# Kernel optimization log

Measured on AMD Instinct MI355X. Metric: run time of the kernel, lower is better.

The kernel has to match this reference:

```python
import jax, jax.numpy as jnp
import numpy as np

B, NQ, HW, C, H = 4, 1024, 4096, 1024, 8
DH = C // H  # 128


def setup_inputs() -> dict:
    key = jax.random.key(0)
    ks = jax.random.split(key, 11)
    s = 0.02
    return {
        "query": jax.random.normal(ks[0], (B, NQ, C), dtype=jnp.float32),
        "memory": jax.random.normal(ks[1], (B, HW, C), dtype=jnp.float32),
        "mask": jax.random.uniform(ks[2], (B, NQ, HW), dtype=jnp.float32),
        "Wq": jax.random.normal(ks[3], (C, C), dtype=jnp.float32) * s,
        "bq": jnp.zeros((C,), dtype=jnp.float32),
        "Wk": jax.random.normal(ks[4], (C, C), dtype=jnp.float32) * s,
        "bk": jnp.zeros((C,), dtype=jnp.float32),
        "Wv": jax.random.normal(ks[5], (C, C), dtype=jnp.float32) * s,
        "bv": jnp.zeros((C,), dtype=jnp.float32),
        "Wo": jax.random.normal(ks[6], (C, C), dtype=jnp.float32) * s,
        "bo": jnp.zeros((C,), dtype=jnp.float32),
    }


def reference(query, memory, mask, Wq, bq, Wk, bk, Wv, bv, Wo, bo):
    # Projections (torch nn.Linear convention: x @ W.T + b)
    q = (query @ Wq.T + bq).reshape(B, NQ, H, DH)
    k = (memory @ Wk.T + bk).reshape(B, HW, H, DH)
    v = (memory @ Wv.T + bv).reshape(B, HW, H, DH)

    scale = 1.0 / jnp.sqrt(jnp.asarray(DH, dtype=q.dtype))
    scores = jnp.einsum("bqhd,bkhd->bhqk", q * scale, k)  # [B,H,NQ,HW]

    # mask < 0.5 means disallowed (True in torch bool attn_mask -> -inf)
    allowed = (mask >= 0.5)[:, None, :, :]  # broadcast over heads
    scores = jnp.where(allowed, scores, jnp.asarray(-jnp.inf, dtype=scores.dtype))

    attn = jax.nn.softmax(scores, axis=-1)
    out = jnp.einsum("bhqk,bkhd->bqhd", attn, v).reshape(B, NQ, C)
    return out @ Wo.T + bo
```

## Files before the change

### kernel.cpp

```cpp
#include <hip/hip_runtime.h>


#define NB 4
#define NQL 1024
#define HWK 4096
#define CC 1024
#define NH 8
#define DHD 128

typedef __attribute__((ext_vector_type(8))) short s16x8;
typedef __attribute__((ext_vector_type(4))) short s16x4;
typedef __attribute__((ext_vector_type(4))) float f32x4;
typedef unsigned int u32;
typedef unsigned long long u64;
typedef const __attribute__((address_space(1))) u32* gas1;
typedef __attribute__((address_space(3))) u32* las3;

__device__ __forceinline__ unsigned short f2bf(float f) {
  u32 u = __float_as_uint(f);
  u32 r = u + 0x7FFFu + ((u >> 16) & 1u);
  return (unsigned short)(r >> 16);
}

__device__ __forceinline__ void gld16(const void* g, void* l) {
  __builtin_amdgcn_global_load_lds((gas1)g, (las3)l, 16, 0, 0);
}

#define MFMA16(a, b, c) __builtin_amdgcn_mfma_f32_16x16x32_bf16((a), (b), (c), 0, 0, 0)

__global__ void cvt_bf16(const float* __restrict__ s, short* __restrict__ d, int n8) {
  int i = blockIdx.x * 256 + threadIdx.x;
  int stride = gridDim.x * 256;
  for (; i < n8; i += stride) {
    const float4* s4 = (const float4*)s;
    float4 a = s4[i * 2];
    float4 b = s4[i * 2 + 1];
    s16x8 o;
    o[0] = (short)f2bf(a.x); o[1] = (short)f2bf(a.y);
    o[2] = (short)f2bf(a.z); o[3] = (short)f2bf(a.w);
    o[4] = (short)f2bf(b.x); o[5] = (short)f2bf(b.y);
    o[6] = (short)f2bf(b.z); o[7] = (short)f2bf(b.w);
    *(s16x8*)(d + (size_t)i * 8) = o;
  }
}

__global__ void mask_bits(const float* __restrict__ mask, u64* __restrict__ words) {
  int t = blockIdx.x * 256 + threadIdx.x;
  int wi = t >> 6;
  int lane = t & 63;
  int k = ((lane >> 2) & 3) * 16 + (lane >> 4) * 4 + (lane & 3);
  float v = mask[(size_t)wi * 64 + k];
  u64 bits = __ballot(v >= 0.5f);
  if (lane == 0) words[wi] = bits;
}

template <int EPI>
__global__ __launch_bounds__(256, 2) void gemm_bt(const short* __restrict__ A,
                                                  const short* __restrict__ W,
                                                  const float* __restrict__ bias,
                                                  void* __restrict__ Cout, float scale) {
  __shared__ alignas(16) short As[128 * 32];
  __shared__ alignas(16) short Bs[128 * 32];
  int nwg = gridDim.x;
  int bid = blockIdx.x;
  int wg = (bid & 7) * (nwg >> 3) + (bid >> 3);
  int bm = wg >> 3;
  int bn = wg & 7;
  int tid = threadIdx.x;
  int w = tid >> 6, lane = tid & 63, lo = lane & 15, hi = lane >> 4;
  int wr = w >> 1, wc = w & 1;
  const short* Ab = A + (size_t)bm * 128 * 1024;
  const short* Wb = W + (size_t)bn * 128 * 1024;
  f32x4 acc[4][4] = {};
  int srow = lane >> 2;
  int scolb = (lane & 3) * 16;

  for (int kt = 0; kt < 32; ++kt) {
    __syncthreads();
#pragma unroll
    for (int i = 0; i < 2; ++i) {
      int c = w * 2 + i;
      int row = c * 16 + srow;
      int sc = scolb ^ ((row & 3) << 4);
      gld16(Ab + (size_t)row * 1024 + kt * 32 + (sc >> 1), (char*)As + c * 1024);
      gld16(Wb + (size_t)row * 1024 + kt * 32 + (sc >> 1), (char*)Bs + c * 1024);
    }
    __syncthreads();
    s16x8 af[4], bf[4];
#pragma unroll
    for (int mf = 0; mf < 4; ++mf) {
      int row = wr * 64 + mf * 16 + lo;
      af[mf] = *(const s16x8*)((const char*)As + row * 64 + ((hi * 16) ^ ((row & 3) << 4)));
    }
#pragma unroll
    for (int nf = 0; nf < 4; ++nf) {
      int row = wc * 64 + nf * 16 + lo;
      bf[nf] = *(const s16x8*)((const char*)Bs + row * 64 + ((hi * 16) ^ ((row & 3) << 4)));
    }
#pragma unroll
    for (int mf = 0; mf < 4; ++mf)
#pragma unroll
      for (int nf = 0; nf < 4; ++nf) acc[mf][nf] = MFMA16(af[mf], bf[nf], acc[mf][nf]);
  }

#pragma unroll
  for (int nf = 0; nf < 4; ++nf) {
    int n = bn * 128 + wc * 64 + nf * 16 + lo;
    float bv = bias[n];
#pragma unroll
    for (int mf = 0; mf < 4; ++mf) {
      int m0 = bm * 128 + wr * 64 + mf * 16 + hi * 4;
      if constexpr (EPI == 0 || EPI == 1) {
        short* O = (short*)Cout;
#pragma unroll
        for (int r = 0; r < 4; ++r) {
          float v = acc[mf][nf][r] + bv;
          if constexpr (EPI == 0) v *= scale;
          O[(size_t)(m0 + r) * 1024 + n] = (short)f2bf(v);
        }
      } else if constexpr (EPI == 2) {
        short* O = (short*)Cout;
        int bb = m0 >> 12;
        int kk = m0 & 4095;
        s16x4 pk;
#pragma unroll
        for (int r = 0; r < 4; ++r) pk[r] = (short)f2bf(acc[mf][nf][r] + bv);
        *(s16x4*)(O + (size_t)bb * 4194304 + (size_t)n * 4096 + kk) = pk;
      } else {
        float* O = (float*)Cout;
#pragma unroll
        for (int r = 0; r < 4; ++r) O[(size_t)(m0 + r) * 1024 + n] = acc[mf][nf][r] + bv;
      }
    }
  }
}

__global__ __launch_bounds__(256, 1) void attn_kernel(const short* __restrict__ Qp,
                                                      const short* __restrict__ Kp,
                                                      const short* __restrict__ VT,
                                                      const u64* __restrict__ Mb,
                                                      short* __restrict__ AO) {
  __shared__ alignas(16) short Ks[2][8192];
  __shared__ alignas(16) short Vs[2][8192];
  __shared__ alignas(16) short Ps[4][2048];

  int bid = blockIdx.x;
  int wg = (bid & 7) * 32 + (bid >> 3);
  int bh = wg >> 3, qb = wg & 7;
  int b = bh >> 3, h = bh & 7;
  int tid = threadIdx.x, w = tid >> 6, lane = tid & 63, lo = lane & 15, hi = lane >> 4;
  int q0 = qb * 128 + w * 32;

  s16x8 qf_[2][4];
#pragma unroll
  for (int qf = 0; qf < 2; ++qf)
#pragma unroll
    for (int kf = 0; kf < 4; ++kf) {
      int q = q0 + qf * 16 + lo;
      qf_[qf][kf] = *(const s16x8*)(Qp + (size_t)(b * NQL + q) * CC + h * DHD + kf * 32 + hi * 8);
    }

  f32x4 acc[2][8] = {};
  float m_[2] = {-3e38f, -3e38f};
  float l_[2] = {0.f, 0.f};

  int krow = lane >> 4;
  int kcolb = (lane & 15) * 16;
  int vrow = lane >> 3;
  int vcolb = (lane & 7) * 16;

  auto stage = [&](int t, int buf) {
    int kv0 = t * 64;
#pragma unroll
    for (int i = 0; i < 4; ++i) {
      int c = w * 4 + i;
      int row = c * 4 + krow;
      int sc = kcolb ^ ((row & 7) << 4);
      gld16(Kp + (size_t)(b * HWK + kv0 + row) * CC + h * DHD + (sc >> 1), (char*)Ks[buf] + c * 1024);
    }
#pragma unroll
    for (int i = 0; i < 4; ++i) {
      int c = w * 4 + i;
      int d = c * 8 + vrow;
      int sc = vcolb ^ ((d & 7) << 4);
      gld16(VT + (size_t)((b * NH + h) * DHD + d) * HWK + kv0 + (sc >> 1), (char*)Vs[buf] + c * 1024);
    }
  };

  stage(0, 0);
  __syncthreads();

  for (int t = 0; t < 64; ++t) {
    int buf = t & 1;
    if (t < 63) stage(t + 1, buf ^ 1);

    f32x4 st[2][4] = {};
#pragma unroll
    for (int nf = 0; nf < 4; ++nf) {
      int kidx = nf * 16 + lo;
      int swz = (kidx & 7) << 4;
#pragma unroll
      for (int kf = 0; kf < 4; ++kf) {
        s16x8 a = *(const s16x8*)((const char*)Ks[buf] + kidx * 256 + ((kf * 64 + hi * 16) ^ swz));
        st[0][nf] = MFMA16(a, qf_[0][kf], st[0][nf]);
        st[1][nf] = MFMA16(a, qf_[1][kf], st[1][nf]);
      }
    }

#pragma unroll
    for (int qf = 0; qf < 2; ++qf) {
      int q = q0 + qf * 16 + lo;
      u64 word = Mb[(size_t)(b * NQL + q) * 64 + t];
      u32 halfm = (u32)(word >> (hi * 16)) & 0xFFFFu;
      float smax = -3e38f;
#pragma unroll
      for (int nf = 0; nf < 4; ++nf)
#pragma unroll
        for (int r = 0; r < 4; ++r) smax = fmaxf(smax, st[qf][nf][r]);
      smax = fmaxf(smax, __shfl_xor(smax, 16));
      smax = fmaxf(smax, __shfl_xor(smax, 32));
      float mnew = fmaxf(m_[qf], smax);
      float alpha = __builtin_amdgcn_exp2f(m_[qf] - mnew);
      float tsum = 0.f;
      int qr = qf * 16 + lo;
#pragma unroll
      for (int nf = 0; nf < 4; ++nf) {
        float p0 = __builtin_amdgcn_exp2f(st[qf][nf][0] - mnew);
        float p1 = __builtin_amdgcn_exp2f(st[qf][nf][1] - mnew);
        float p2 = __builtin_amdgcn_exp2f(st[qf][nf][2] - mnew);
        float p3 = __builtin_amdgcn_exp2f(st[qf][nf][3] - mnew);
        p0 = ((halfm >> (nf * 4 + 0)) & 1) ? p0 : 0.f;
        p1 = ((halfm >> (nf * 4 + 1)) & 1) ? p1 : 0.f;
        p2 = ((halfm >> (nf * 4 + 2)) & 1) ? p2 : 0.f;
        p3 = ((halfm >> (nf * 4 + 3)) & 1) ? p3 : 0.f;
        tsum += p0 + p1 + p2 + p3;
        u32 w0 = __builtin_amdgcn_perm(__float_as_uint(p1), __float_as_uint(p0), 0x07060302u);
        u32 w1 = __builtin_amdgcn_perm(__float_as_uint(p3), __float_as_uint(p2), 0x07060302u);
        uint2 pv; pv.x = w0; pv.y = w1;
        *(uint2*)((char*)Ps[w] + qr * 128 + ((nf * 32 + hi * 8) ^ ((lo & 7) << 4))) = pv;
      }
      tsum += __shfl_xor(tsum, 16);
      tsum += __shfl_xor(tsum, 32);
      l_[qf] = l_[qf] * alpha + tsum;
      m_[qf] = mnew;
      float ar0 = __shfl(alpha, hi * 4 + 0);
      float ar1 = __shfl(alpha, hi * 4 + 1);
      float ar2 = __shfl(alpha, hi * 4 + 2);
      float ar3 = __shfl(alpha, hi * 4 + 3);
#pragma unroll
      for (int df = 0; df < 8; ++df) {
        acc[qf][df][0] *= ar0; acc[qf][df][1] *= ar1;
        acc[qf][df][2] *= ar2; acc[qf][df][3] *= ar3;
      }
    }
    asm volatile("" ::: "memory");

#pragma unroll
    for (int kt = 0; kt < 2; ++kt) {
      s16x8 pa0 = *(const s16x8*)((const char*)Ps[w] + (0 + lo) * 128 + ((kt * 64 + hi * 16) ^ ((lo & 7) << 4)));
      s16x8 pa1 = *(const s16x8*)((const char*)Ps[w] + (16 + lo) * 128 + ((kt * 64 + hi * 16) ^ ((lo & 7) << 4)));
#pragma unroll
      for (int df = 0; df < 8; ++df) {
        int d = df * 16 + lo;
        s16x8 vb = *(const s16x8*)((const char*)Vs[buf] + d * 128 + ((kt * 64 + hi * 16) ^ ((lo & 7) << 4)));
        acc[0][df] = MFMA16(pa0, vb, acc[0][df]);
        acc[1][df] = MFMA16(pa1, vb, acc[1][df]);
      }
    }
    __syncthreads();
  }

#pragma unroll
  for (int qf = 0; qf < 2; ++qf) {
    float linv = 1.0f / l_[qf];
    float lr0 = __shfl(linv, hi * 4 + 0);
    float lr1 = __shfl(linv, hi * 4 + 1);
    float lr2 = __shfl(linv, hi * 4 + 2);
    float lr3 = __shfl(linv, hi * 4 + 3);
    int qbase = q0 + qf * 16 + hi * 4;
#pragma unroll
    for (int df = 0; df < 8; ++df) {
      int col = h * DHD + df * 16 + lo;
      AO[(size_t)(b * NQL + qbase + 0) * CC + col] = (short)f2bf(acc[qf][df][0] * lr0);
      AO[(size_t)(b * NQL + qbase + 1) * CC + col] = (short)f2bf(acc[qf][df][1] * lr1);
      AO[(size_t)(b * NQL + qbase + 2) * CC + col] = (short)f2bf(acc[qf][df][2] * lr2);
      AO[(size_t)(b * NQL + qbase + 3) * CC + col] = (short)f2bf(acc[qf][df][3] * lr3);
    }
  }
}

extern "C" void kernel_launch(void* const* d_in, const int* in_sizes, int n_in,
                              void* d_out, int out_size, void* d_ws, size_t ws_size,
                              hipStream_t stream) {
  (void)in_sizes; (void)n_in; (void)out_size; (void)ws_size;
  const float* query = (const float*)d_in[0];
  const float* memory = (const float*)d_in[1];
  const float* mask = (const float*)d_in[2];
  const float* Wq = (const float*)d_in[3];
  const float* bq = (const float*)d_in[4];
  const float* Wk = (const float*)d_in[5];
  const float* bk = (const float*)d_in[6];
  const float* Wv = (const float*)d_in[7];
  const float* bv = (const float*)d_in[8];
  const float* Wo = (const float*)d_in[9];
  const float* bo = (const float*)d_in[10];
  float* out = (float*)d_out;

  char* ws = (char*)d_ws;
  short* qbf = (short*)(ws);
  short* mbf = (short*)(ws + (8ull << 20));
  short* wqb = (short*)(ws + (40ull << 20));
  short* wkb = wqb + (1u << 20);
  short* wvb = wqb + (2u << 20);
  short* wob = wqb + (3u << 20);
  u64* mbits = (u64*)(ws + (48ull << 20));
  short* Qp = (short*)(ws + (50ull << 20));
  short* Kp = (short*)(ws + (58ull << 20));
  short* VT = (short*)(ws + (90ull << 20));
  short* AO = (short*)(ws + (122ull << 20));

  cvt_bf16<<<2048, 256, 0, stream>>>(query, qbf, (NB * NQL * CC) / 8);
  cvt_bf16<<<2048, 256, 0, stream>>>(memory, mbf, (NB * HWK * CC) / 8);
  cvt_bf16<<<512, 256, 0, stream>>>(Wq, wqb, (CC * CC) / 8);
  cvt_bf16<<<512, 256, 0, stream>>>(Wk, wkb, (CC * CC) / 8);
  cvt_bf16<<<512, 256, 0, stream>>>(Wv, wvb, (CC * CC) / 8);
  cvt_bf16<<<512, 256, 0, stream>>>(Wo, wob, (CC * CC) / 8);
  mask_bits<<<65536, 256, 0, stream>>>(mask, mbits);

  const float qscale = 0.08838834764831845f * 1.4426950408889634f;
  gemm_bt<0><<<256, 256, 0, stream>>>(qbf, wqb, bq, Qp, qscale);
  gemm_bt<1><<<1024, 256, 0, stream>>>(mbf, wkb, bk, Kp, 1.0f);
  gemm_bt<2><<<1024, 256, 0, stream>>>(mbf, wvb, bv, VT, 1.0f);
  attn_kernel<<<256, 256, 0, stream>>>(Qp, Kp, VT, mbits, AO);
  gemm_bt<3><<<256, 256, 0, stream>>>(AO, wob, bo, out, 1.0f);
}
```

Baseline: 525.2 us.

## Halve attention query tile per block to double occupancy, add lazy rescale

Each wave of the attention kernel now handles 16 query rows instead of 32, and the grid doubles to 512 blocks with launch bounds allowing two blocks per CU. The aim is more waves in flight across 256 CUs, so memory latency and the softmax phase can overlap with other blocks' MFMA work. It also rescales the accumulator only when the running max grows by more than 8 (in log2 units), and raises wave priority around the MFMA sections. The cost is that every K/V tile loaded from memory is reused by half as many queries, which doubles K/V traffic, and the loose max threshold lets the unnormalized probabilities grow up to 2^8.

```diff
diff --git a/kernel.cpp b/kernel.cpp
--- a/kernel.cpp
+++ b/kernel.cpp
@@ -135,34 +135,31 @@
   }
 }
 
-__global__ __launch_bounds__(256, 1) void attn_kernel(const short* __restrict__ Qp,
+__global__ __launch_bounds__(256, 2) void attn_kernel(const short* __restrict__ Qp,
                                                       const short* __restrict__ Kp,
                                                       const short* __restrict__ VT,
                                                       const u64* __restrict__ Mb,
                                                       short* __restrict__ AO) {
   __shared__ alignas(16) short Ks[2][8192];
   __shared__ alignas(16) short Vs[2][8192];
-  __shared__ alignas(16) short Ps[4][2048];
+  __shared__ alignas(16) short Ps[4][1024];
 
   int bid = blockIdx.x;
-  int wg = (bid & 7) * 32 + (bid >> 3);
-  int bh = wg >> 3, qb = wg & 7;
+  int wg = (bid & 7) * 64 + (bid >> 3);
+  int bh = wg >> 4, qb = wg & 15;
   int b = bh >> 3, h = bh & 7;
   int tid = threadIdx.x, w = tid >> 6, lane = tid & 63, lo = lane & 15, hi = lane >> 4;
-  int q0 = qb * 128 + w * 32;
-
-  s16x8 qf_[2][4];
-#pragma unroll
-  for (int qf = 0; qf < 2; ++qf)
-#pragma unroll
-    for (int kf = 0; kf < 4; ++kf) {
-      int q = q0 + qf * 16 + lo;
-      qf_[qf][kf] = *(const s16x8*)(Qp + (size_t)(b * NQL + q) * CC + h * DHD + kf * 32 + hi * 8);
-    }
-
-  f32x4 acc[2][8] = {};
-  float m_[2] = {-3e38f, -3e38f};
-  float l_[2] = {0.f, 0.f};
+  int q0 = qb * 64 + w * 16;
+  int q = q0 + lo;
+
+  s16x8 qfr[4];
+#pragma unroll
+  for (int kf = 0; kf < 4; ++kf)
+    qfr[kf] = *(const s16x8*)(Qp + (size_t)(b * NQL + q) * CC + h * DHD + kf * 32 + hi * 8);
+
+  f32x4 acc[8] = {};
+  float m_ = -3e38f;
+  float l_ = 0.f;
 
   int krow = lane >> 4;
   int kcolb = (lane & 15) * 16;
@@ -194,7 +191,8 @@
     int buf = t & 1;
     if (t < 63) stage(t + 1, buf ^ 1);
 
-    f32x4 st[2][4] = {};
+    __builtin_amdgcn_s_setprio(1);
+    f32x4 st[4] = {};
 #pragma unroll
     for (int nf = 0; nf < 4; ++nf) {
       int kidx = nf * 16 + lo;
@@ -202,90 +200,87 @@
 #pragma unroll
       for (int kf = 0; kf < 4; ++kf) {
         s16x8 a = *(const s16x8*)((const char*)Ks[buf] + kidx * 256 + ((kf * 64 + hi * 16) ^ swz));
-        st[0][nf] = MFMA16(a, qf_[0][kf], st[0][nf]);
-        st[1][nf] = MFMA16(a, qf_[1][kf], st[1][nf]);
+        st[nf] = MFMA16(a, qfr[kf], st[nf]);
       }
     }
-
-#pragma unroll
-    for (int qf = 0; qf < 2; ++qf) {
-      int q = q0 + qf * 16 + lo;
-      u64 word = Mb[(size_t)(b * NQL + q) * 64 + t];
-      u32 halfm = (u32)(word >> (hi * 16)) & 0xFFFFu;
-      float smax = -3e38f;
-#pragma unroll
-      for (int nf = 0; nf < 4; ++nf)
-#pragma unroll
-        for (int r = 0; r < 4; ++r) smax = fmaxf(smax, st[qf][nf][r]);
-      smax = fmaxf(smax, __shfl_xor(smax, 16));
-      smax = fmaxf(smax, __shfl_xor(smax, 32));
-      float mnew = fmaxf(m_[qf], smax);
-      float alpha = __builtin_amdgcn_exp2f(m_[qf] - mnew);
-      float tsum = 0.f;
-      int qr = qf * 16 + lo;
-#pragma unroll
-      for (int nf = 0; nf < 4; ++nf) {
-        float p0 = __builtin_amdgcn_exp2f(st[qf][nf][0] - mnew);
-        float p1 = __builtin_amdgcn_exp2f(st[qf][nf][1] - mnew);
-        float p2 = __builtin_amdgcn_exp2f(st[qf][nf][2] - mnew);
-        float p3 = __builtin_amdgcn_exp2f(st[qf][nf][3] - mnew);
-        p0 = ((halfm >> (nf * 4 + 0)) & 1) ? p0 : 0.f;
-        p1 = ((halfm >> (nf * 4 + 1)) & 1) ? p1 : 0.f;
-        p2 = ((halfm >> (nf * 4 + 2)) & 1) ? p2 : 0.f;
-        p3 = ((halfm >> (nf * 4 + 3)) & 1) ? p3 : 0.f;
-        tsum += p0 + p1 + p2 + p3;
-        u32 w0 = __builtin_amdgcn_perm(__float_as_uint(p1), __float_as_uint(p0), 0x07060302u);
-        u32 w1 = __builtin_amdgcn_perm(__float_as_uint(p3), __float_as_uint(p2), 0x07060302u);
-        uint2 pv; pv.x = w0; pv.y = w1;
-        *(uint2*)((char*)Ps[w] + qr * 128 + ((nf * 32 + hi * 8) ^ ((lo & 7) << 4))) = pv;
-      }
-      tsum += __shfl_xor(tsum, 16);
-      tsum += __shfl_xor(tsum, 32);
-      l_[qf] = l_[qf] * alpha + tsum;
-      m_[qf] = mnew;
+    __builtin_amdgcn_s_setprio(0);
+
+    u64 word = Mb[(size_t)(b * NQL + q) * 64 + t];
+    u32 halfm = (u32)(word >> (hi * 16)) & 0xFFFFu;
+    float smax = -3e38f;
+#pragma unroll
+    for (int nf = 0; nf < 4; ++nf)
+#pragma unroll
+      for (int r = 0; r < 4; ++r) smax = fmaxf(smax, st[nf][r]);
+    smax = fmaxf(smax, __shfl_xor(smax, 16));
+    smax = fmaxf(smax, __shfl_xor(smax, 32));
+
+    if (__any(smax > m_ + 8.f)) {
+      float mnew = fmaxf(m_, smax);
+      float alpha = __builtin_amdgcn_exp2f(m_ - mnew);
+      l_ *= alpha;
+      m_ = mnew;
       float ar0 = __shfl(alpha, hi * 4 + 0);
       float ar1 = __shfl(alpha, hi * 4 + 1);
       float ar2 = __shfl(alpha, hi * 4 + 2);
       float ar3 = __shfl(alpha, hi * 4 + 3);
 #pragma unroll
       for (int df = 0; df < 8; ++df) {
-        acc[qf][df][0] *= ar0; acc[qf][df][1] *= ar1;
-        acc[qf][df][2] *= ar2; acc[qf][df][3] *= ar3;
+        acc[df][0] *= ar0; acc[df][1] *= ar1;
+        acc[df][2] *= ar2; acc[df][3] *= ar3;
       }
     }
+
+    float tsum = 0.f;
+#pragma unroll
+    for (int nf = 0; nf < 4; ++nf) {
+      float p0 = __builtin_amdgcn_exp2f(st[nf][0] - m_);
+      float p1 = __builtin_amdgcn_exp2f(st[nf][1] - m_);
+      float p2 = __builtin_amdgcn_exp2f(st[nf][2] - m_);
+      float p3 = __builtin_amdgcn_exp2f(st[nf][3] - m_);
+      p0 = ((halfm >> (nf * 4 + 0)) & 1) ? p0 : 0.f;
+      p1 = ((halfm >> (nf * 4 + 1)) & 1) ? p1 : 0.f;
+      p2 = ((halfm >> (nf * 4 + 2)) & 1) ? p2 : 0.f;
+      p3 = ((halfm >> (nf * 4 + 3)) & 1) ? p3 : 0.f;
+      tsum += p0 + p1 + p2 + p3;
+      u32 w0 = __builtin_amdgcn_perm(__float_as_uint(p1), __float_as_uint(p0), 0x07060302u);
+      u32 w1 = __builtin_amdgcn_perm(__float_as_uint(p3), __float_as_uint(p2), 0x07060302u);
+      uint2 pv; pv.x = w0; pv.y = w1;
+      *(uint2*)((char*)Ps[w] + lo * 128 + ((nf * 32 + hi * 8) ^ ((lo & 7) << 4))) = pv;
+    }
+    tsum += __shfl_xor(tsum, 16);
+    tsum += __shfl_xor(tsum, 32);
+    l_ += tsum;
     asm volatile("" ::: "memory");
 
+    __builtin_amdgcn_s_setprio(1);
 #pragma unroll
     for (int kt = 0; kt < 2; ++kt) {
-      s16x8 pa0 = *(const s16x8*)((const char*)Ps[w] + (0 + lo) * 128 + ((kt * 64 + hi * 16) ^ ((lo & 7) << 4)));
-      s16x8 pa1 = *(const s16x8*)((const char*)Ps[w] + (16 + lo) * 128 + ((kt * 64 + hi * 16) ^ ((lo & 7) << 4)));
+      s16x8 pa = *(const s16x8*)((const char*)Ps[w] + lo * 128 + ((kt * 64 + hi * 16) ^ ((lo & 7) << 4)));
 #pragma unroll
       for (int df = 0; df < 8; ++df) {
         int d = df * 16 + lo;
         s16x8 vb = *(const s16x8*)((const char*)Vs[buf] + d * 128 + ((kt * 64 + hi * 16) ^ ((lo & 7) << 4)));
-        acc[0][df] = MFMA16(pa0, vb, acc[0][df]);
-        acc[1][df] = MFMA16(pa1, vb, acc[1][df]);
+        acc[df] = MFMA16(pa, vb, acc[df]);
       }
     }
+    __builtin_amdgcn_s_setprio(0);
     __syncthreads();
   }
 
-#pragma unroll
-  for (int qf = 0; qf < 2; ++qf) {
-    float linv = 1.0f / l_[qf];
-    float lr0 = __shfl(linv, hi * 4 + 0);
-    float lr1 = __shfl(linv, hi * 4 + 1);
-    float lr2 = __shfl(linv, hi * 4 + 2);
-    float lr3 = __shfl(linv, hi * 4 + 3);
-    int qbase = q0 + qf * 16 + hi * 4;
-#pragma unroll
-    for (int df = 0; df < 8; ++df) {
-      int col = h * DHD + df * 16 + lo;
-      AO[(size_t)(b * NQL + qbase + 0) * CC + col] = (short)f2bf(acc[qf][df][0] * lr0);
-      AO[(size_t)(b * NQL + qbase + 1) * CC + col] = (short)f2bf(acc[qf][df][1] * lr1);
-      AO[(size_t)(b * NQL + qbase + 2) * CC + col] = (short)f2bf(acc[qf][df][2] * lr2);
-      AO[(size_t)(b * NQL + qbase + 3) * CC + col] = (short)f2bf(acc[qf][df][3] * lr3);
-    }
+  float linv = 1.0f / l_;
+  float lr0 = __shfl(linv, hi * 4 + 0);
+  float lr1 = __shfl(linv, hi * 4 + 1);
+  float lr2 = __shfl(linv, hi * 4 + 2);
+  float lr3 = __shfl(linv, hi * 4 + 3);
+  int qbase = q0 + hi * 4;
+#pragma unroll
+  for (int df = 0; df < 8; ++df) {
+    int col = h * DHD + df * 16 + lo;
+    AO[(size_t)(b * NQL + qbase + 0) * CC + col] = (short)f2bf(acc[df][0] * lr0);
+    AO[(size_t)(b * NQL + qbase + 1) * CC + col] = (short)f2bf(acc[df][1] * lr1);
+    AO[(size_t)(b * NQL + qbase + 2) * CC + col] = (short)f2bf(acc[df][2] * lr2);
+    AO[(size_t)(b * NQL + qbase + 3) * CC + col] = (short)f2bf(acc[df][3] * lr3);
   }
 }
 
@@ -331,6 +326,6 @@
   gemm_bt<0><<<256, 256, 0, stream>>>(qbf, wqb, bq, Qp, qscale);
   gemm_bt<1><<<1024, 256, 0, stream>>>(mbf, wkb, bk, Kp, 1.0f);
   gemm_bt<2><<<1024, 256, 0, stream>>>(mbf, wvb, bv, VT, 1.0f);
-  attn_kernel<<<256, 256, 0, stream>>>(Qp, Kp, VT, mbits, AO);
+  attn_kernel<<<512, 256, 0, stream>>>(Qp, Kp, VT, mbits, AO);
   gemm_bt<3><<<256, 256, 0, stream>>>(AO, wob, bo, out, 1.0f);
 }
```

Measured after the change: 459.4 us. 12.5% less time.
